# Kernel tuning notes

Hardware: AMD Instinct MI355X
Metric: run time of the kernel (lower is better)

The kernel has to match this reference:

```python
import jax, jax.numpy as jnp
import numpy as np

DIM = 1024
N_HEADS = 16
HEAD_DIM = 64


def setup_inputs() -> dict:
    key = jax.random.key(0)
    kx, kq, kk, kv, ko = jax.random.split(key, 5)
    B, T = 4, 2048
    s = DIM ** -0.5  # roughly torch Linear init scale
    return {
        "x": jax.random.normal(kx, (B, T, DIM), dtype=jnp.float32),
        "Wq": jax.random.normal(kq, (DIM, DIM), dtype=jnp.float32) * s,
        "Wk": jax.random.normal(kk, (DIM, DIM), dtype=jnp.float32) * s,
        "Wv": jax.random.normal(kv, (DIM, DIM), dtype=jnp.float32) * s,
        "Wo": jax.random.normal(ko, (DIM, DIM), dtype=jnp.float32) * s,
    }


def reference(x, Wq, Wk, Wv, Wo):
    B, T, D = x.shape
    h, hd = N_HEADS, HEAD_DIM
    # torch nn.Linear: y = x @ W.T
    q = (x @ Wq.T).reshape(B, T, h, hd).transpose(0, 2, 1, 3)  # [B,h,T,hd]
    k = (x @ Wk.T).reshape(B, T, h, hd).transpose(0, 2, 1, 3)
    v = (x @ Wv.T).reshape(B, T, h, hd).transpose(0, 2, 1, 3)
    scale = hd ** -0.5
    # The torch loop over query chunks with full-K softmax is mathematically
    # identical to full (non-causal) softmax attention.
    scores = jnp.einsum("bhqd,bhkd->bhqk", q, k) * scale  # [B,h,T,T]
    attn = jax.nn.softmax(scores, axis=-1)
    out = jnp.einsum("bhqk,bhkd->bhqd", attn, v)  # [B,h,T,hd]
    out = out.transpose(0, 2, 1, 3).reshape(B, T, D)
    return out @ Wo.T
```

## Files before the change

kernel.cpp:

```cpp
#include <hip/hip_runtime.h>

typedef float f32x4 __attribute__((ext_vector_type(4)));
typedef float f32x16 __attribute__((ext_vector_type(16)));
typedef short s16x8 __attribute__((ext_vector_type(8)));
typedef unsigned int u32x4 __attribute__((ext_vector_type(4)));

#define B_SZ 4
#define T_SZ 2048
#define D_SZ 1024
#define NH 16
#define HD 64
#define KVB 64

#define CLQ (0.125f * 1.44269504089f)

__device__ __forceinline__ unsigned short f2b(float f) {
  unsigned int u = __builtin_bit_cast(unsigned int, f);
  unsigned int r = (u + 0x7fffu + ((u >> 16) & 1u)) >> 16;
  return (unsigned short)r;
}

__device__ __forceinline__ void gld_lds16(void* lds, const void* g) {
  __builtin_amdgcn_global_load_lds(
      (const __attribute__((address_space(1))) unsigned int*)g,
      (__attribute__((address_space(3))) unsigned int*)lds, 16, 0, 0);
}

__device__ __forceinline__ float vsum16(f32x16 v) {
  float t0 = (v[0] + v[1]) + (v[2] + v[3]);
  float t1 = (v[4] + v[5]) + (v[6] + v[7]);
  float t2 = (v[8] + v[9]) + (v[10] + v[11]);
  float t3 = (v[12] + v[13]) + (v[14] + v[15]);
  return (t0 + t1) + (t2 + t3);
}

__global__ void cast_kernel(const float* __restrict__ in,
                            unsigned short* __restrict__ out, int n4) {
  int i = blockIdx.x * blockDim.x + threadIdx.x;
  if (i < n4) {
    float4 v = reinterpret_cast<const float4*>(in)[i];
    ushort4 o;
    o.x = f2b(v.x); o.y = f2b(v.y); o.z = f2b(v.z); o.w = f2b(v.w);
    reinterpret_cast<ushort4*>(out)[i] = o;
  }
}

__global__ void cast_w4(const float* __restrict__ w0, const float* __restrict__ w1,
                        const float* __restrict__ w2, const float* __restrict__ w3,
                        unsigned short* __restrict__ o0, unsigned short* __restrict__ o1,
                        unsigned short* __restrict__ o2, unsigned short* __restrict__ o3) {
  int i = blockIdx.x * blockDim.x + threadIdx.x;
  const int w = i >> 18, j = i & 262143;
  const float* src = (w == 0) ? w0 : (w == 1) ? w1 : (w == 2) ? w2 : w3;
  unsigned short* dst = (w == 0) ? o0 : (w == 1) ? o1 : (w == 2) ? o2 : o3;
  float4 v = reinterpret_cast<const float4*>(src)[j];
  ushort4 o;
  o.x = f2b(v.x); o.y = f2b(v.y); o.z = f2b(v.z); o.w = f2b(v.w);
  reinterpret_cast<ushort4*>(dst)[j] = o;
}

#define BM 128
#define BN 128
#define BKG 64

template <int MODE>
__global__ __launch_bounds__(256, 2) void gemm_bt(
    const unsigned short* __restrict__ A,
    const unsigned short* __restrict__ W,
    void* __restrict__ Cv, int M, int N, int K) {
  __shared__ __align__(16) char As[BM * 128];
  __shared__ __align__(16) char Ws[BN * 128];
  const int tid = threadIdx.x, wid = tid >> 6, lane = tid & 63;
  const int row0 = blockIdx.x * BM, col0 = blockIdx.y * BN;
  const int wr = (wid >> 1) * 64, wc = (wid & 1) * 64;
  const int fr = lane & 15;
  const int kgB = (lane >> 4) * 16;
  f32x4 acc[4][4] = {};

  const int srow = lane >> 3;
  const int sc = lane & 7;
  const int sch = sc ^ srow;

  for (int k0 = 0; k0 < K; k0 += BKG) {
    __syncthreads();
#pragma unroll
    for (int i = 0; i < 4; ++i) {
      const int c = wid + 4 * i;
      const int row = c * 8 + srow;
      gld_lds16(As + c * 1024, &A[(row0 + row) * K + k0 + sch * 8]);
      gld_lds16(Ws + c * 1024, &W[(col0 + row) * K + k0 + sch * 8]);
    }
    __syncthreads();
    s16x8 af[4][2], bf[4][2];
#pragma unroll
    for (int m = 0; m < 4; ++m) {
      const int row = wr + m * 16 + fr;
#pragma unroll
      for (int kk = 0; kk < 2; ++kk)
        af[m][kk] = *(const s16x8*)(As + row * 128 + ((kk * 64 + kgB) ^ ((row & 7) << 4)));
    }
#pragma unroll
    for (int n = 0; n < 4; ++n) {
      const int row = wc + n * 16 + fr;
#pragma unroll
      for (int kk = 0; kk < 2; ++kk)
        bf[n][kk] = *(const s16x8*)(Ws + row * 128 + ((kk * 64 + kgB) ^ ((row & 7) << 4)));
    }
#pragma unroll
    for (int kk = 0; kk < 2; ++kk)
#pragma unroll
      for (int m = 0; m < 4; ++m)
#pragma unroll
        for (int n = 0; n < 4; ++n)
          acc[m][n] = __builtin_amdgcn_mfma_f32_16x16x32_bf16(af[m][kk], bf[n][kk], acc[m][n], 0, 0, 0);
  }

  const int crow = row0 + wr + ((lane >> 4) << 2);
  const int ccol = col0 + wc + fr;
#pragma unroll
  for (int m = 0; m < 4; ++m)
#pragma unroll
    for (int n = 0; n < 4; ++n) {
      if constexpr (MODE == 2) {
        unsigned short* C = (unsigned short*)Cv;
        ushort4 pk;
        pk.x = f2b(acc[m][n][0]); pk.y = f2b(acc[m][n][1]);
        pk.z = f2b(acc[m][n][2]); pk.w = f2b(acc[m][n][3]);
        const int tok = crow + m * 16;
        const int c = ccol + n * 16;
        *(ushort4*)&C[((tok >> 11) * 1024 + c) * 2048 + (tok & 2047)] = pk;
      } else {
#pragma unroll
        for (int r = 0; r < 4; ++r) {
          float v = acc[m][n][r];
          if constexpr (MODE == 3) v *= CLQ;
          const int idx = (crow + m * 16 + r) * N + ccol + n * 16;
          if constexpr (MODE == 1)
            ((float*)Cv)[idx] = v;
          else
            ((unsigned short*)Cv)[idx] = f2b(v);
        }
      }
    }
}

__global__ __launch_bounds__(256, 2) void attn_kernel(
    const unsigned short* __restrict__ Q,
    const unsigned short* __restrict__ K,
    const unsigned short* __restrict__ Vt,
    unsigned short* __restrict__ O) {
  __shared__ __align__(16) char Kl[2][KVB * 128];
  __shared__ __align__(16) char Vl[2][HD * 128];

  const int tid = threadIdx.x, wid = tid >> 6, lane = tid & 63;
  const int ql = lane & 31;
  const int hi = lane >> 5;
  const int srow = lane >> 3;
  const int sc = lane & 7;

  const int lin = blockIdx.y * gridDim.x + blockIdx.x;
  const int work = (lin & 7) * 64 + (lin >> 3);
  const int qc = work & 7, bh = work >> 3;
  const int b = bh >> 4, h = bh & 15;
  const int q0 = qc * 256 + wid * 64;
  const int qkbase = b * T_SZ * D_SZ + h * HD;
  const int vtbase = (b * D_SZ + h * HD) * T_SZ;

  auto STAGE = [&](int bufi, int kv0) {
#pragma unroll
    for (int i = 0; i < 2; ++i) {
      const int c = wid + 4 * i;
      const int row = c * 8 + srow;
      const int sch = sc ^ (row & 7);
      gld_lds16(Kl[bufi] + c * 1024, &K[qkbase + (kv0 + row) * D_SZ + sch * 8]);
      gld_lds16(Vl[bufi] + c * 1024, &Vt[vtbase + row * T_SZ + kv0 + sch * 8]);
    }
  };

  s16x8 qf[2][4];
#pragma unroll
  for (int c = 0; c < 2; ++c)
#pragma unroll
    for (int kq = 0; kq < 4; ++kq)
      qf[c][kq] = *(const s16x8*)&Q[qkbase + (q0 + c * 32 + ql) * D_SZ + kq * 16 + hi * 8];

  f32x16 ot[2][2] = {};
  float l[2] = {0.f, 0.f};

  STAGE(0, 0);
  int cur = 0;

#pragma unroll 1
  for (int kv0 = 0; kv0 < T_SZ; kv0 += KVB) {
    const int kvn = (kv0 + KVB) & (T_SZ - 1);
    __syncthreads();
    STAGE(cur ^ 1, kvn);

    const char* Kb = Kl[cur];
    const char* Vb = Vl[cur];

    s16x8 vfr[4][2];
#pragma unroll
    for (int ks = 0; ks < 4; ++ks)
#pragma unroll
      for (int dblk = 0; dblk < 2; ++dblk) {
        const int vr = dblk * 32 + ql;
        vfr[ks][dblk] = *(const s16x8*)(Vb + vr * 128 +
                          ((ks * 32 + hi * 16) ^ ((vr & 7) << 4)));
      }

    f32x16 st[2][2] = {};
#pragma unroll
    for (int blk = 0; blk < 2; ++blk)
#pragma unroll
      for (int kq = 0; kq < 4; ++kq) {
        const int kr = blk * 32 + ql;
        const s16x8 k8 = *(const s16x8*)(Kb + kr * 128 +
                           ((kq * 32 + hi * 16) ^ ((kr & 7) << 4)));
#pragma unroll
        for (int c = 0; c < 2; ++c)
          st[c][blk] = __builtin_amdgcn_mfma_f32_32x32x16_bf16(k8, qf[c][kq], st[c][blk], 0, 0, 0);
      }

#pragma unroll
    for (int c = 0; c < 2; ++c) {
#pragma unroll
      for (int blk = 0; blk < 2; ++blk)
#pragma unroll
        for (int r = 0; r < 16; ++r)
          st[c][blk][r] = __builtin_amdgcn_exp2f(st[c][blk][r]);
      l[c] += vsum16(st[c][0]) + vsum16(st[c][1]);
    }

#pragma unroll
    for (int c = 0; c < 2; ++c) {
      s16x8 pf[4];
#pragma unroll
      for (int ks = 0; ks < 4; ++ks) {
        const int blk = ks >> 1, rb = (ks & 1) * 8;
        unsigned int a0, a1, b0, b1;
        asm("v_cvt_pk_bf16_f32 %0, %1, %2" : "=v"(a0) : "v"(st[c][blk][rb + 0]), "v"(st[c][blk][rb + 1]));
        asm("v_cvt_pk_bf16_f32 %0, %1, %2" : "=v"(a1) : "v"(st[c][blk][rb + 2]), "v"(st[c][blk][rb + 3]));
        asm("v_cvt_pk_bf16_f32 %0, %1, %2" : "=v"(b0) : "v"(st[c][blk][rb + 4]), "v"(st[c][blk][rb + 5]));
        asm("v_cvt_pk_bf16_f32 %0, %1, %2" : "=v"(b1) : "v"(st[c][blk][rb + 6]), "v"(st[c][blk][rb + 7]));
        asm("v_permlane32_swap_b32 %0, %1" : "+v"(a0), "+v"(b0));
        asm("v_permlane32_swap_b32 %0, %1" : "+v"(a1), "+v"(b1));
        u32x4 w = {a0, a1, b0, b1};
        pf[ks] = __builtin_bit_cast(s16x8, w);
      }
#pragma unroll
      for (int ks = 0; ks < 4; ++ks)
#pragma unroll
        for (int dblk = 0; dblk < 2; ++dblk)
          ot[c][dblk] = __builtin_amdgcn_mfma_f32_32x32x16_bf16(vfr[ks][dblk], pf[ks], ot[c][dblk], 0, 0, 0);
    }

    cur ^= 1;
  }

#pragma unroll
  for (int c = 0; c < 2; ++c) {
    const float lt = l[c] + __shfl_xor(l[c], 32, 64);
    const float inv = 1.f / lt;
    const int orow = qkbase + (q0 + c * 32 + ql) * D_SZ;
#pragma unroll
    for (int dblk = 0; dblk < 2; ++dblk)
#pragma unroll
      for (int qd = 0; qd < 4; ++qd) {
        ushort4 pk;
        pk.x = f2b(ot[c][dblk][qd * 4 + 0] * inv);
        pk.y = f2b(ot[c][dblk][qd * 4 + 1] * inv);
        pk.z = f2b(ot[c][dblk][qd * 4 + 2] * inv);
        pk.w = f2b(ot[c][dblk][qd * 4 + 3] * inv);
        *(ushort4*)&O[orow + dblk * 32 + qd * 8 + hi * 4] = pk;
      }
  }
}

extern "C" void kernel_launch(void* const* d_in, const int* in_sizes, int n_in,
                              void* d_out, int out_size, void* d_ws, size_t ws_size,
                              hipStream_t stream) {
  const float* x  = (const float*)d_in[0];
  const float* Wq = (const float*)d_in[1];
  const float* Wk = (const float*)d_in[2];
  const float* Wv = (const float*)d_in[3];
  const float* Wo = (const float*)d_in[4];

  const int NTOK = B_SZ * T_SZ;
  const int SZX = NTOK * D_SZ;
  const int SZW = D_SZ * D_SZ;

  unsigned short* ws  = (unsigned short*)d_ws;
  unsigned short* xb  = ws;
  unsigned short* wqb = xb + SZX;
  unsigned short* wkb = wqb + SZW;
  unsigned short* wvb = wkb + SZW;
  unsigned short* wob = wvb + SZW;
  unsigned short* Qb  = wob + SZW;
  unsigned short* Kb  = Qb + SZX;
  unsigned short* Vtb = Kb + SZX;

  cast_kernel<<<SZX / 1024, 256, 0, stream>>>(x, xb, SZX / 4);
  cast_w4<<<4 * (SZW / 4) / 256, 256, 0, stream>>>(Wq, Wk, Wv, Wo, wqb, wkb, wvb, wob);

  dim3 gg(NTOK / BM, D_SZ / BN);
  gemm_bt<3><<<gg, 256, 0, stream>>>(xb, wqb, Qb, NTOK, D_SZ, D_SZ);
  gemm_bt<0><<<gg, 256, 0, stream>>>(xb, wkb, Kb, NTOK, D_SZ, D_SZ);
  gemm_bt<2><<<gg, 256, 0, stream>>>(xb, wvb, Vtb, NTOK, D_SZ, D_SZ);

  dim3 ga(T_SZ / 256, B_SZ * NH);
  attn_kernel<<<ga, 256, 0, stream>>>(Qb, Kb, Vtb, xb);

  gemm_bt<1><<<gg, 256, 0, stream>>>(xb, wob, (float*)d_out, NTOK, D_SZ, D_SZ);
}
```

Before: 182.2 us.

## Shrink attention query tile per wave and drop LDS double buffering

The attention kernel now handles 32 query rows per wave (128 per block) instead of 64, and the grid doubles to 1024 blocks. The K/V staging becomes single-buffered with a sync before and after each load, and launch bounds rise to 3 blocks per CU. The goal is higher occupancy and more blocks to spread across CUs. In exchange, each K/V tile loaded into LDS is reused by half as many queries, and global-to-LDS loads no longer overlap with compute.

Result: slower. 189.8 us (+4.1%).

```diff
diff --git a/kernel.cpp b/kernel.cpp
--- a/kernel.cpp
+++ b/kernel.cpp
@@ -144,13 +144,13 @@
     }
 }
 
-__global__ __launch_bounds__(256, 2) void attn_kernel(
+__global__ __launch_bounds__(256, 3) void attn_kernel(
     const unsigned short* __restrict__ Q,
     const unsigned short* __restrict__ K,
     const unsigned short* __restrict__ Vt,
     unsigned short* __restrict__ O) {
-  __shared__ __align__(16) char Kl[2][KVB * 128];
-  __shared__ __align__(16) char Vl[2][HD * 128];
+  __shared__ __align__(16) char Kl[KVB * 128];
+  __shared__ __align__(16) char Vl[HD * 128];
 
   const int tid = threadIdx.x, wid = tid >> 6, lane = tid & 63;
   const int ql = lane & 31;
@@ -159,45 +159,33 @@
   const int sc = lane & 7;
 
   const int lin = blockIdx.y * gridDim.x + blockIdx.x;
-  const int work = (lin & 7) * 64 + (lin >> 3);
-  const int qc = work & 7, bh = work >> 3;
+  const int work = (lin & 7) * 128 + (lin >> 3);
+  const int qc = work & 15, bh = work >> 4;
   const int b = bh >> 4, h = bh & 15;
-  const int q0 = qc * 256 + wid * 64;
+  const int q0 = qc * 128 + wid * 32;
   const int qkbase = b * T_SZ * D_SZ + h * HD;
   const int vtbase = (b * D_SZ + h * HD) * T_SZ;
 
-  auto STAGE = [&](int bufi, int kv0) {
+  s16x8 qf[4];
+#pragma unroll
+  for (int kq = 0; kq < 4; ++kq)
+    qf[kq] = *(const s16x8*)&Q[qkbase + (q0 + ql) * D_SZ + kq * 16 + hi * 8];
+
+  f32x16 ot[2] = {};
+  float l = 0.f;
+
+#pragma unroll 1
+  for (int kv0 = 0; kv0 < T_SZ; kv0 += KVB) {
+    __syncthreads();
 #pragma unroll
     for (int i = 0; i < 2; ++i) {
       const int c = wid + 4 * i;
       const int row = c * 8 + srow;
       const int sch = sc ^ (row & 7);
-      gld_lds16(Kl[bufi] + c * 1024, &K[qkbase + (kv0 + row) * D_SZ + sch * 8]);
-      gld_lds16(Vl[bufi] + c * 1024, &Vt[vtbase + row * T_SZ + kv0 + sch * 8]);
-    }
-  };
-
-  s16x8 qf[2][4];
-#pragma unroll
-  for (int c = 0; c < 2; ++c)
-#pragma unroll
-    for (int kq = 0; kq < 4; ++kq)
-      qf[c][kq] = *(const s16x8*)&Q[qkbase + (q0 + c * 32 + ql) * D_SZ + kq * 16 + hi * 8];
-
-  f32x16 ot[2][2] = {};
-  float l[2] = {0.f, 0.f};
-
-  STAGE(0, 0);
-  int cur = 0;
-
-#pragma unroll 1
-  for (int kv0 = 0; kv0 < T_SZ; kv0 += KVB) {
-    const int kvn = (kv0 + KVB) & (T_SZ - 1);
-    __syncthreads();
-    STAGE(cur ^ 1, kvn);
-
-    const char* Kb = Kl[cur];
-    const char* Vb = Vl[cur];
+      gld_lds16(Kl + c * 1024, &K[qkbase + (kv0 + row) * D_SZ + sch * 8]);
+      gld_lds16(Vl + c * 1024, &Vt[vtbase + row * T_SZ + kv0 + sch * 8]);
+    }
+    __syncthreads();
 
     s16x8 vfr[4][2];
 #pragma unroll
@@ -205,76 +193,63 @@
 #pragma unroll
       for (int dblk = 0; dblk < 2; ++dblk) {
         const int vr = dblk * 32 + ql;
-        vfr[ks][dblk] = *(const s16x8*)(Vb + vr * 128 +
+        vfr[ks][dblk] = *(const s16x8*)(Vl + vr * 128 +
                           ((ks * 32 + hi * 16) ^ ((vr & 7) << 4)));
       }
 
-    f32x16 st[2][2] = {};
+    f32x16 st[2] = {};
 #pragma unroll
     for (int blk = 0; blk < 2; ++blk)
 #pragma unroll
       for (int kq = 0; kq < 4; ++kq) {
         const int kr = blk * 32 + ql;
-        const s16x8 k8 = *(const s16x8*)(Kb + kr * 128 +
+        const s16x8 k8 = *(const s16x8*)(Kl + kr * 128 +
                            ((kq * 32 + hi * 16) ^ ((kr & 7) << 4)));
-#pragma unroll
-        for (int c = 0; c < 2; ++c)
-          st[c][blk] = __builtin_amdgcn_mfma_f32_32x32x16_bf16(k8, qf[c][kq], st[c][blk], 0, 0, 0);
+        st[blk] = __builtin_amdgcn_mfma_f32_32x32x16_bf16(k8, qf[kq], st[blk], 0, 0, 0);
       }
 
 #pragma unroll
-    for (int c = 0; c < 2; ++c) {
-#pragma unroll
-      for (int blk = 0; blk < 2; ++blk)
-#pragma unroll
-        for (int r = 0; r < 16; ++r)
-          st[c][blk][r] = __builtin_amdgcn_exp2f(st[c][blk][r]);
-      l[c] += vsum16(st[c][0]) + vsum16(st[c][1]);
-    }
-
-#pragma unroll
-    for (int c = 0; c < 2; ++c) {
-      s16x8 pf[4];
-#pragma unroll
-      for (int ks = 0; ks < 4; ++ks) {
-        const int blk = ks >> 1, rb = (ks & 1) * 8;
-        unsigned int a0, a1, b0, b1;
-        asm("v_cvt_pk_bf16_f32 %0, %1, %2" : "=v"(a0) : "v"(st[c][blk][rb + 0]), "v"(st[c][blk][rb + 1]));
-        asm("v_cvt_pk_bf16_f32 %0, %1, %2" : "=v"(a1) : "v"(st[c][blk][rb + 2]), "v"(st[c][blk][rb + 3]));
-        asm("v_cvt_pk_bf16_f32 %0, %1, %2" : "=v"(b0) : "v"(st[c][blk][rb + 4]), "v"(st[c][blk][rb + 5]));
-        asm("v_cvt_pk_bf16_f32 %0, %1, %2" : "=v"(b1) : "v"(st[c][blk][rb + 6]), "v"(st[c][blk][rb + 7]));
-        asm("v_permlane32_swap_b32 %0, %1" : "+v"(a0), "+v"(b0));
-        asm("v_permlane32_swap_b32 %0, %1" : "+v"(a1), "+v"(b1));
-        u32x4 w = {a0, a1, b0, b1};
-        pf[ks] = __builtin_bit_cast(s16x8, w);
-      }
-#pragma unroll
-      for (int ks = 0; ks < 4; ++ks)
-#pragma unroll
-        for (int dblk = 0; dblk < 2; ++dblk)
-          ot[c][dblk] = __builtin_amdgcn_mfma_f32_32x32x16_bf16(vfr[ks][dblk], pf[ks], ot[c][dblk], 0, 0, 0);
-    }
-
-    cur ^= 1;
+    for (int blk = 0; blk < 2; ++blk)
+#pragma unroll
+      for (int r = 0; r < 16; ++r)
+        st[blk][r] = __builtin_amdgcn_exp2f(st[blk][r]);
+    l += vsum16(st[0]) + vsum16(st[1]);
+
+    s16x8 pf[4];
+#pragma unroll
+    for (int ks = 0; ks < 4; ++ks) {
+      const int blk = ks >> 1, rb = (ks & 1) * 8;
+      unsigned int a0, a1, b0, b1;
+      asm("v_cvt_pk_bf16_f32 %0, %1, %2" : "=v"(a0) : "v"(st[blk][rb + 0]), "v"(st[blk][rb + 1]));
+      asm("v_cvt_pk_bf16_f32 %0, %1, %2" : "=v"(a1) : "v"(st[blk][rb + 2]), "v"(st[blk][rb + 3]));
+      asm("v_cvt_pk_bf16_f32 %0, %1, %2" : "=v"(b0) : "v"(st[blk][rb + 4]), "v"(st[blk][rb + 5]));
+      asm("v_cvt_pk_bf16_f32 %0, %1, %2" : "=v"(b1) : "v"(st[blk][rb + 6]), "v"(st[blk][rb + 7]));
+      asm("v_permlane32_swap_b32 %0, %1" : "+v"(a0), "+v"(b0));
+      asm("v_permlane32_swap_b32 %0, %1" : "+v"(a1), "+v"(b1));
+      u32x4 w = {a0, a1, b0, b1};
+      pf[ks] = __builtin_bit_cast(s16x8, w);
+    }
+#pragma unroll
+    for (int ks = 0; ks < 4; ++ks)
+#pragma unroll
+      for (int dblk = 0; dblk < 2; ++dblk)
+        ot[dblk] = __builtin_amdgcn_mfma_f32_32x32x16_bf16(vfr[ks][dblk], pf[ks], ot[dblk], 0, 0, 0);
   }
 
-#pragma unroll
-  for (int c = 0; c < 2; ++c) {
-    const float lt = l[c] + __shfl_xor(l[c], 32, 64);
-    const float inv = 1.f / lt;
-    const int orow = qkbase + (q0 + c * 32 + ql) * D_SZ;
-#pragma unroll
-    for (int dblk = 0; dblk < 2; ++dblk)
-#pragma unroll
-      for (int qd = 0; qd < 4; ++qd) {
-        ushort4 pk;
-        pk.x = f2b(ot[c][dblk][qd * 4 + 0] * inv);
-        pk.y = f2b(ot[c][dblk][qd * 4 + 1] * inv);
-        pk.z = f2b(ot[c][dblk][qd * 4 + 2] * inv);
-        pk.w = f2b(ot[c][dblk][qd * 4 + 3] * inv);
-        *(ushort4*)&O[orow + dblk * 32 + qd * 8 + hi * 4] = pk;
-      }
-  }
+  const float lt = l + __shfl_xor(l, 32, 64);
+  const float inv = 1.f / lt;
+  const int orow = qkbase + (q0 + ql) * D_SZ;
+#pragma unroll
+  for (int dblk = 0; dblk < 2; ++dblk)
+#pragma unroll
+    for (int qd = 0; qd < 4; ++qd) {
+      ushort4 pk;
+      pk.x = f2b(ot[dblk][qd * 4 + 0] * inv);
+      pk.y = f2b(ot[dblk][qd * 4 + 1] * inv);
+      pk.z = f2b(ot[dblk][qd * 4 + 2] * inv);
+      pk.w = f2b(ot[dblk][qd * 4 + 3] * inv);
+      *(ushort4*)&O[orow + dblk * 32 + qd * 8 + hi * 4] = pk;
+    }
 }
 
 extern "C" void kernel_launch(void* const* d_in, const int* in_sizes, int n_in,
@@ -308,7 +283,7 @@
   gemm_bt<0><<<gg, 256, 0, stream>>>(xb, wkb, Kb, NTOK, D_SZ, D_SZ);
   gemm_bt<2><<<gg, 256, 0, stream>>>(xb, wvb, Vtb, NTOK, D_SZ, D_SZ);
 
-  dim3 ga(T_SZ / 256, B_SZ * NH);
+  dim3 ga(T_SZ / 128, B_SZ * NH);
   attn_kernel<<<ga, 256, 0, stream>>>(Qb, Kb, Vtb, xb);
 
   gemm_bt<1><<<gg, 256, 0, stream>>>(xb, wob, (float*)d_out, NTOK, D_SZ, D_SZ);
```

## Fuse QKV projections into one launch and single-buffer attention K/V staging

Applied to the files above, without the earlier changes.

Merges the three Q/K/V projection GEMMs into one kernel that picks its weight matrix and output layout from blockIdx.y, so one larger grid replaces three launches. The attention kernel drops its double-buffered K/V LDS staging in favour of a single buffer, loaded and synchronised before compute on each KV block. This halves LDS use but removes the overlap between global-to-LDS loads and MFMA work, exposing load latency each iteration.

Result: faster. 165.1 us (-9.4%).

```diff
diff --git a/kernel.cpp b/kernel.cpp
--- a/kernel.cpp
+++ b/kernel.cpp
@@ -63,11 +63,94 @@
 #define BN 128
 #define BKG 64
 
-template <int MODE>
-__global__ __launch_bounds__(256, 2) void gemm_bt(
+__global__ __launch_bounds__(256, 2) void gemm_qkv(
+    const unsigned short* __restrict__ A,
+    const unsigned short* __restrict__ Wq,
+    const unsigned short* __restrict__ Wk,
+    const unsigned short* __restrict__ Wv,
+    unsigned short* __restrict__ Qo,
+    unsigned short* __restrict__ Ko,
+    unsigned short* __restrict__ Vto) {
+  __shared__ __align__(16) char As[BM * 128];
+  __shared__ __align__(16) char Ws[BN * 128];
+  const int tid = threadIdx.x, wid = tid >> 6, lane = tid & 63;
+  const int sel = blockIdx.y >> 3;
+  const unsigned short* W = (sel == 0) ? Wq : (sel == 1) ? Wk : Wv;
+  const int row0 = blockIdx.x * BM, col0 = (blockIdx.y & 7) * BN;
+  const int wr = (wid >> 1) * 64, wc = (wid & 1) * 64;
+  const int fr = lane & 15;
+  const int kgB = (lane >> 4) * 16;
+  f32x4 acc[4][4] = {};
+
+  const int srow = lane >> 3;
+  const int sc = lane & 7;
+  const int sch = sc ^ srow;
+
+  for (int k0 = 0; k0 < D_SZ; k0 += BKG) {
+    __syncthreads();
+#pragma unroll
+    for (int i = 0; i < 4; ++i) {
+      const int c = wid + 4 * i;
+      const int row = c * 8 + srow;
+      gld_lds16(As + c * 1024, &A[(row0 + row) * D_SZ + k0 + sch * 8]);
+      gld_lds16(Ws + c * 1024, &W[(col0 + row) * D_SZ + k0 + sch * 8]);
+    }
+    __syncthreads();
+    s16x8 af[4][2], bf[4][2];
+#pragma unroll
+    for (int m = 0; m < 4; ++m) {
+      const int row = wr + m * 16 + fr;
+#pragma unroll
+      for (int kk = 0; kk < 2; ++kk)
+        af[m][kk] = *(const s16x8*)(As + row * 128 + ((kk * 64 + kgB) ^ ((row & 7) << 4)));
+    }
+#pragma unroll
+    for (int n = 0; n < 4; ++n) {
+      const int row = wc + n * 16 + fr;
+#pragma unroll
+      for (int kk = 0; kk < 2; ++kk)
+        bf[n][kk] = *(const s16x8*)(Ws + row * 128 + ((kk * 64 + kgB) ^ ((row & 7) << 4)));
+    }
+#pragma unroll
+    for (int kk = 0; kk < 2; ++kk)
+#pragma unroll
+      for (int m = 0; m < 4; ++m)
+#pragma unroll
+        for (int n = 0; n < 4; ++n)
+          acc[m][n] = __builtin_amdgcn_mfma_f32_16x16x32_bf16(af[m][kk], bf[n][kk], acc[m][n], 0, 0, 0);
+  }
+
+  const int crow = row0 + wr + ((lane >> 4) << 2);
+  const int ccol = col0 + wc + fr;
+  if (sel == 2) {
+#pragma unroll
+    for (int m = 0; m < 4; ++m)
+#pragma unroll
+      for (int n = 0; n < 4; ++n) {
+        ushort4 pk;
+        pk.x = f2b(acc[m][n][0]); pk.y = f2b(acc[m][n][1]);
+        pk.z = f2b(acc[m][n][2]); pk.w = f2b(acc[m][n][3]);
+        const int tok = crow + m * 16;
+        const int c = ccol + n * 16;
+        *(ushort4*)&Vto[((tok >> 11) * 1024 + c) * 2048 + (tok & 2047)] = pk;
+      }
+  } else {
+    unsigned short* C = (sel == 0) ? Qo : Ko;
+    const float s = (sel == 0) ? CLQ : 1.0f;
+#pragma unroll
+    for (int m = 0; m < 4; ++m)
+#pragma unroll
+      for (int n = 0; n < 4; ++n)
+#pragma unroll
+        for (int r = 0; r < 4; ++r)
+          C[(crow + m * 16 + r) * D_SZ + ccol + n * 16] = f2b(acc[m][n][r] * s);
+  }
+}
+
+__global__ __launch_bounds__(256, 2) void gemm_out(
     const unsigned short* __restrict__ A,
     const unsigned short* __restrict__ W,
-    void* __restrict__ Cv, int M, int N, int K) {
+    float* __restrict__ C, int M, int N, int K) {
   __shared__ __align__(16) char As[BM * 128];
   __shared__ __align__(16) char Ws[BN * 128];
   const int tid = threadIdx.x, wid = tid >> 6, lane = tid & 63;
@@ -120,28 +203,10 @@
 #pragma unroll
   for (int m = 0; m < 4; ++m)
 #pragma unroll
-    for (int n = 0; n < 4; ++n) {
-      if constexpr (MODE == 2) {
-        unsigned short* C = (unsigned short*)Cv;
-        ushort4 pk;
-        pk.x = f2b(acc[m][n][0]); pk.y = f2b(acc[m][n][1]);
-        pk.z = f2b(acc[m][n][2]); pk.w = f2b(acc[m][n][3]);
-        const int tok = crow + m * 16;
-        const int c = ccol + n * 16;
-        *(ushort4*)&C[((tok >> 11) * 1024 + c) * 2048 + (tok & 2047)] = pk;
-      } else {
-#pragma unroll
-        for (int r = 0; r < 4; ++r) {
-          float v = acc[m][n][r];
-          if constexpr (MODE == 3) v *= CLQ;
-          const int idx = (crow + m * 16 + r) * N + ccol + n * 16;
-          if constexpr (MODE == 1)
-            ((float*)Cv)[idx] = v;
-          else
-            ((unsigned short*)Cv)[idx] = f2b(v);
-        }
-      }
-    }
+    for (int n = 0; n < 4; ++n)
+#pragma unroll
+      for (int r = 0; r < 4; ++r)
+        C[(crow + m * 16 + r) * N + ccol + n * 16] = acc[m][n][r];
 }
 
 __global__ __launch_bounds__(256, 2) void attn_kernel(
@@ -149,8 +214,8 @@
     const unsigned short* __restrict__ K,
     const unsigned short* __restrict__ Vt,
     unsigned short* __restrict__ O) {
-  __shared__ __align__(16) char Kl[2][KVB * 128];
-  __shared__ __align__(16) char Vl[2][HD * 128];
+  __shared__ __align__(16) char Kl[KVB * 128];
+  __shared__ __align__(16) char Vl[HD * 128];
 
   const int tid = threadIdx.x, wid = tid >> 6, lane = tid & 63;
   const int ql = lane & 31;
@@ -166,38 +231,28 @@
   const int qkbase = b * T_SZ * D_SZ + h * HD;
   const int vtbase = (b * D_SZ + h * HD) * T_SZ;
 
-  auto STAGE = [&](int bufi, int kv0) {
+  s16x8 qf[2][4];
+#pragma unroll
+  for (int c = 0; c < 2; ++c)
+#pragma unroll
+    for (int kq = 0; kq < 4; ++kq)
+      qf[c][kq] = *(const s16x8*)&Q[qkbase + (q0 + c * 32 + ql) * D_SZ + kq * 16 + hi * 8];
+
+  f32x16 ot[2][2] = {};
+  float l[2] = {0.f, 0.f};
+
+#pragma unroll 1
+  for (int kv0 = 0; kv0 < T_SZ; kv0 += KVB) {
+    __syncthreads();
 #pragma unroll
     for (int i = 0; i < 2; ++i) {
       const int c = wid + 4 * i;
       const int row = c * 8 + srow;
       const int sch = sc ^ (row & 7);
-      gld_lds16(Kl[bufi] + c * 1024, &K[qkbase + (kv0 + row) * D_SZ + sch * 8]);
-      gld_lds16(Vl[bufi] + c * 1024, &Vt[vtbase + row * T_SZ + kv0 + sch * 8]);
-    }
-  };
-
-  s16x8 qf[2][4];
-#pragma unroll
-  for (int c = 0; c < 2; ++c)
-#pragma unroll
-    for (int kq = 0; kq < 4; ++kq)
-      qf[c][kq] = *(const s16x8*)&Q[qkbase + (q0 + c * 32 + ql) * D_SZ + kq * 16 + hi * 8];
-
-  f32x16 ot[2][2] = {};
-  float l[2] = {0.f, 0.f};
-
-  STAGE(0, 0);
-  int cur = 0;
-
-#pragma unroll 1
-  for (int kv0 = 0; kv0 < T_SZ; kv0 += KVB) {
-    const int kvn = (kv0 + KVB) & (T_SZ - 1);
-    __syncthreads();
-    STAGE(cur ^ 1, kvn);
-
-    const char* Kb = Kl[cur];
-    const char* Vb = Vl[cur];
+      gld_lds16(Kl + c * 1024, &K[qkbase + (kv0 + row) * D_SZ + sch * 8]);
+      gld_lds16(Vl + c * 1024, &Vt[vtbase + row * T_SZ + kv0 + sch * 8]);
+    }
+    __syncthreads();
 
     s16x8 vfr[4][2];
 #pragma unroll
@@ -205,7 +260,7 @@
 #pragma unroll
       for (int dblk = 0; dblk < 2; ++dblk) {
         const int vr = dblk * 32 + ql;
-        vfr[ks][dblk] = *(const s16x8*)(Vb + vr * 128 +
+        vfr[ks][dblk] = *(const s16x8*)(Vl + vr * 128 +
                           ((ks * 32 + hi * 16) ^ ((vr & 7) << 4)));
       }
 
@@ -215,7 +270,7 @@
 #pragma unroll
       for (int kq = 0; kq < 4; ++kq) {
         const int kr = blk * 32 + ql;
-        const s16x8 k8 = *(const s16x8*)(Kb + kr * 128 +
+        const s16x8 k8 = *(const s16x8*)(Kl + kr * 128 +
                            ((kq * 32 + hi * 16) ^ ((kr & 7) << 4)));
 #pragma unroll
         for (int c = 0; c < 2; ++c)
@@ -254,8 +309,6 @@
         for (int dblk = 0; dblk < 2; ++dblk)
           ot[c][dblk] = __builtin_amdgcn_mfma_f32_32x32x16_bf16(vfr[ks][dblk], pf[ks], ot[c][dblk], 0, 0, 0);
     }
-
-    cur ^= 1;
   }
 
 #pragma unroll
@@ -303,13 +356,12 @@
   cast_kernel<<<SZX / 1024, 256, 0, stream>>>(x, xb, SZX / 4);
   cast_w4<<<4 * (SZW / 4) / 256, 256, 0, stream>>>(Wq, Wk, Wv, Wo, wqb, wkb, wvb, wob);
 
-  dim3 gg(NTOK / BM, D_SZ / BN);
-  gemm_bt<3><<<gg, 256, 0, stream>>>(xb, wqb, Qb, NTOK, D_SZ, D_SZ);
-  gemm_bt<0><<<gg, 256, 0, stream>>>(xb, wkb, Kb, NTOK, D_SZ, D_SZ);
-  gemm_bt<2><<<gg, 256, 0, stream>>>(xb, wvb, Vtb, NTOK, D_SZ, D_SZ);
+  dim3 gq(NTOK / BM, 24);
+  gemm_qkv<<<gq, 256, 0, stream>>>(xb, wqb, wkb, wvb, Qb, Kb, Vtb);
 
   dim3 ga(T_SZ / 256, B_SZ * NH);
   attn_kernel<<<ga, 256, 0, stream>>>(Qb, Kb, Vtb, xb);
 
-  gemm_bt<1><<<gg, 256, 0, stream>>>(xb, wob, (float*)d_out, NTOK, D_SZ, D_SZ);
-}
+  dim3 gg(NTOK / BM, D_SZ / BN);
+  gemm_out<<<gg, 256, 0, stream>>>(xb, wob, (float*)d_out, NTOK, D_SZ, D_SZ);
+}
```
